# Performance work log

Measured on AMD Instinct MI355X. Metric: run time of the kernel, lower is better.

## Reference

```python
import jax, jax.numpy as jnp
import numpy as np
from jax import lax

B, T_IN, T_OUT = 32, 400, 500
N_MEL, ENC, RNN, PRE, ATT, LOC_F, LOC_K = 80, 512, 1024, 256, 128, 32, 31


def setup_inputs() -> dict:
    key = jax.random.key(0)
    ks = jax.random.split(key, 16)
    s = 0.02
    p = lambda i, sh: (jax.random.normal(ks[i], sh) * s).astype(jnp.float32)
    memory = jax.random.normal(ks[0], (B, T_IN, ENC), dtype=jnp.float32)
    decoder_inputs = jax.random.normal(ks[1], (B, N_MEL, T_OUT), dtype=jnp.float32)
    memory_lengths = jax.random.randint(ks[2], (B,), T_IN // 2, T_IN + 1).at[0].set(T_IN).astype(jnp.int32)
    return {
        'memory': memory,
        'decoder_inputs': decoder_inputs,
        'memory_lengths': memory_lengths,
        'prenet_w1': p(3, (PRE, N_MEL)),
        'prenet_w2': p(4, (PRE, PRE)),
        'att_wih': p(5, (4 * RNN, PRE + ENC)),
        'att_whh': p(6, (4 * RNN, RNN)),
        'att_bih': jnp.zeros((4 * RNN,), jnp.float32),
        'att_bhh': jnp.zeros((4 * RNN,), jnp.float32),
        'query_w': p(7, (ATT, RNN)),
        'memory_w': p(8, (ATT, ENC)),
        'v_w': p(9, (1, ATT)),
        'loc_conv_w': p(10, (LOC_F, 2, LOC_K)),
        'loc_lin_w': p(11, (ATT, LOC_F)),
        'dec_wih': p(12, (4 * RNN, RNN + ENC)),
        'dec_whh': p(13, (4 * RNN, RNN)),
        'dec_bih': jnp.zeros((4 * RNN,), jnp.float32),
        'dec_bhh': jnp.zeros((4 * RNN,), jnp.float32),
        'proj_w': p(14, (N_MEL, RNN + ENC)),
        'proj_b': jnp.zeros((N_MEL,), jnp.float32),
        'gate_w': p(15, (1, RNN + ENC)),
        'gate_b': jnp.zeros((1,), jnp.float32),
    }


def _lstm(x, h, c, wih, whh, bih, bhh):
    g = x @ wih.T + h @ whh.T + bih + bhh
    i, f, gg, o = jnp.split(g, 4, axis=-1)
    c2 = jax.nn.sigmoid(f) * c + jax.nn.sigmoid(i) * jnp.tanh(gg)
    return jax.nn.sigmoid(o) * jnp.tanh(c2), c2


def _forward(memory, decoder_inputs, memory_lengths, prenet_w1, prenet_w2,
             att_wih, att_whh, att_bih, att_bhh, query_w, memory_w, v_w,
             loc_conv_w, loc_lin_w, dec_wih, dec_whh, dec_bih, dec_bhh,
             proj_w, proj_b, gate_w, gate_b):
    # deterministic dropout masks (prenet p=0.5 always on; rnn dropout p=0.1, training mode)
    k1, k2, k3, k4 = jax.random.split(jax.random.key(42), 4)
    # teacher-forced inputs: [B,80,T_out] -> [T_out,B,80], prepend all-zero go frame
    dec_in = jnp.transpose(decoder_inputs, (2, 0, 1))
    dec_in = jnp.concatenate([jnp.zeros((1, B, N_MEL), decoder_inputs.dtype), dec_in], axis=0)
    x = dec_in
    for w, k in ((prenet_w1, k1), (prenet_w2, k2)):
        x = jax.nn.relu(x @ w.T)
        x = jnp.where(jax.random.bernoulli(k, 0.5, x.shape), x * 2.0, 0.0)
    prenet_out = x[:T_OUT]  # one decode step per target frame
    att_drop = jnp.where(jax.random.bernoulli(k3, 0.9, (T_OUT, B, RNN)), 1.0 / 0.9, 0.0).astype(jnp.float32)
    dec_drop = jnp.where(jax.random.bernoulli(k4, 0.9, (T_OUT, B, RNN)), 1.0 / 0.9, 0.0).astype(jnp.float32)
    processed_memory = memory @ memory_w.T  # [B,T_in,ATT]
    valid = jnp.arange(T_IN)[None, :] < memory_lengths[:, None]  # [B,T_in]
    pad = (LOC_K - 1) // 2

    def step(carry, xs):
        ah, ac, dh, dc, aw, awc, ctx = carry
        din, am, dm = xs
        ah, ac = _lstm(jnp.concatenate([din, ctx], -1), ah, ac, att_wih, att_whh, att_bih, att_bhh)
        ah = ah * am
        cat = jnp.stack([aw, awc], axis=1)  # [B,2,T_in]
        loc = lax.conv_general_dilated(cat, loc_conv_w, (1,), [(pad, pad)], dimension_numbers=('NCH', 'OIH', 'NCH'))
        loc = jnp.einsum('bft,af->bta', loc, loc_lin_w)  # [B,T_in,ATT]
        pq = (ah @ query_w.T)[:, None, :]  # [B,1,ATT]
        e = jnp.tanh(pq + loc + processed_memory) @ v_w[0]  # [B,T_in]
        e = jnp.where(valid, e, -jnp.inf)
        aw2 = jax.nn.softmax(e, axis=1)
        ctx2 = jnp.einsum('bt,btd->bd', aw2, memory)
        awc2 = awc + aw2
        dh, dc = _lstm(jnp.concatenate([ah, ctx2], -1), dh, dc, dec_wih, dec_whh, dec_bih, dec_bhh)
        dh = dh * dm
        hc = jnp.concatenate([dh, ctx2], -1)
        mel = hc @ proj_w.T + proj_b
        gate = (hc @ gate_w.T + gate_b)[:, 0]
        return (ah, ac, dh, dc, aw2, awc2, ctx2), (mel, gate, aw2)

    z = lambda *sh: jnp.zeros(sh, jnp.float32)
    carry0 = (z(B, RNN), z(B, RNN), z(B, RNN), z(B, RNN), z(B, T_IN), z(B, T_IN), z(B, ENC))
    _, (mels, gates, aligns) = lax.scan(step, carry0, (prenet_out, att_drop, dec_drop))
    mel_outputs = jnp.transpose(mels, (1, 2, 0))      # [B, n_mel, T_out]
    gate_outputs = gates.T                             # [B, T_out]
    alignments = jnp.transpose(aligns, (1, 0, 2))      # [B, T_out, T_in]
    return mel_outputs, gate_outputs, alignments


def reference(memory, decoder_inputs, memory_lengths, prenet_w1, prenet_w2,
              att_wih, att_whh, att_bih, att_bhh, query_w, memory_w, v_w,
              loc_conv_w, loc_lin_w, dec_wih, dec_whh, dec_bih, dec_bhh,
              proj_w, proj_b, gate_w, gate_b):
    return _forward(memory, decoder_inputs, memory_lengths, prenet_w1, prenet_w2,
                    att_wih, att_whh, att_bih, att_bhh, query_w, memory_w, v_w,
                    loc_conv_w, loc_lin_w, dec_wih, dec_whh, dec_bih, dec_bhh,
                    proj_w, proj_b, gate_w, gate_b)
```

## Files before the change

kernel.cpp:

```cpp
#include <hip/hip_runtime.h>
#include <cstdint>

typedef unsigned short ushortT;
typedef __attribute__((ext_vector_type(8))) short s8v;
typedef __attribute__((ext_vector_type(4))) float f4v;

#define TIN 400
#define TOUT 500

__host__ __device__ __forceinline__ uint32_t rotl32(uint32_t v, int r){ return (v<<r)|(v>>(32-r)); }
__host__ __device__ inline void tf2x32(uint32_t k0, uint32_t k1, uint32_t x0, uint32_t x1,
                                       uint32_t* o0, uint32_t* o1){
  uint32_t ks2 = k0 ^ k1 ^ 0x1BD11BDAu;
  x0 += k0; x1 += k1;
  x0+=x1; x1=rotl32(x1,13); x1^=x0;  x0+=x1; x1=rotl32(x1,15); x1^=x0;
  x0+=x1; x1=rotl32(x1,26); x1^=x0;  x0+=x1; x1=rotl32(x1, 6); x1^=x0;
  x0+=k1; x1+=ks2+1u;
  x0+=x1; x1=rotl32(x1,17); x1^=x0;  x0+=x1; x1=rotl32(x1,29); x1^=x0;
  x0+=x1; x1=rotl32(x1,16); x1^=x0;  x0+=x1; x1=rotl32(x1,24); x1^=x0;
  x0+=ks2; x1+=k0+2u;
  x0+=x1; x1=rotl32(x1,13); x1^=x0;  x0+=x1; x1=rotl32(x1,15); x1^=x0;
  x0+=x1; x1=rotl32(x1,26); x1^=x0;  x0+=x1; x1=rotl32(x1, 6); x1^=x0;
  x0+=k0; x1+=k1+3u;
  x0+=x1; x1=rotl32(x1,17); x1^=x0;  x0+=x1; x1=rotl32(x1,29); x1^=x0;
  x0+=x1; x1=rotl32(x1,16); x1^=x0;  x0+=x1; x1=rotl32(x1,24); x1^=x0;
  x0+=k1; x1+=ks2+4u;
  x0+=x1; x1=rotl32(x1,13); x1^=x0;  x0+=x1; x1=rotl32(x1,15); x1^=x0;
  x0+=x1; x1=rotl32(x1,26); x1^=x0;  x0+=x1; x1=rotl32(x1, 6); x1^=x0;
  x0+=ks2; x1+=k0+5u;
  *o0 = x0; *o1 = x1;
}
__device__ __forceinline__ float part_unif(uint32_t ka, uint32_t kb, uint32_t idx){
  uint32_t o0,o1; tf2x32(ka,kb,0u,idx,&o0,&o1);
  uint32_t bits = o0 ^ o1;
  return __uint_as_float(0x3f800000u | (bits>>9)) - 1.0f;
}

__device__ __forceinline__ float bf2f(ushortT u){ return __uint_as_float(((uint32_t)u)<<16); }
__device__ __forceinline__ ushortT f2bf(float f){
  uint32_t x = __float_as_uint(f);
  return (ushortT)((x + 0x7fffu + ((x>>16)&1u)) >> 16);
}
__device__ __forceinline__ float sigm(float x){ return 1.0f/(1.0f+__expf(-x)); }
__device__ __forceinline__ f4v mfma16(s8v a, s8v b, f4v c){
  return __builtin_amdgcn_mfma_f32_16x16x32_bf16(a,b,c,0,0,0);
}
__device__ __forceinline__ s8v pack8(const float* p){
  s8v r;
  #pragma unroll
  for (int j=0;j<8;++j) r[j]=(short)f2bf(p[j]);
  return r;
}

__global__ __launch_bounds__(256) void k_setup(
  const float* __restrict__ memory, const float* __restrict__ qw,
  const float* __restrict__ pjw,  const float* __restrict__ gw,
  ushortT* __restrict__ Mbf, ushortT* __restrict__ Wq, ushortT* __restrict__ Wpg,
  ushortT* __restrict__ AH0, ushortT* __restrict__ AH1,
  ushortT* __restrict__ DH0, ushortT* __restrict__ DH1,
  ushortT* __restrict__ CT0, ushortT* __restrict__ CT1,
  float* __restrict__ aw, float* __restrict__ awc,
  uint32_t* __restrict__ bars)
{
  int stride = gridDim.x*blockDim.x;
  int g0 = blockIdx.x*blockDim.x + threadIdx.x;
  for (int i=g0; i<32*400*512; i+=stride) Mbf[i]=f2bf(memory[i]);
  for (int i=g0; i<128*1024;  i+=stride) Wq[i]=f2bf(qw[i]);
  for (int i=g0; i<96*1536; i+=stride){
    int r=i/1536, k=i-r*1536;
    ushortT v=0;
    if (r<80) v=f2bf(pjw[r*1536+k]);
    else if (r==80) v=f2bf(gw[k]);
    Wpg[i]=v;
  }
  for (int i=g0; i<32*1024; i+=stride){ AH0[i]=0; AH1[i]=0; DH0[i]=0; DH1[i]=0; }
  for (int i=g0; i<32*512;  i+=stride){ CT0[i]=0; CT1[i]=0; }
  for (int i=g0; i<32*400;  i+=stride){ aw[i]=0.f; awc[i]=0.f; }
  if (g0 < 8) bars[g0]=0u;
}

__global__ __launch_bounds__(256) void k_prenet(
  const float* __restrict__ dec_inp, const float* __restrict__ w1, const float* __restrict__ w2,
  ushortT* __restrict__ preo,
  uint32_t k1a, uint32_t k1b, uint32_t k2a, uint32_t k2b)
{
  __shared__ ushortT Xs[64*96];
  __shared__ ushortT H1s[64*256];
  int tid=threadIdx.x, lane=tid&63, wv=tid>>6, quad=lane>>4, nl=lane&15;
  int r0 = blockIdx.x*64;
  for (int i=tid; i<64*96; i+=256){
    int rr=i/96, k=i-rr*96; int row=r0+rr; int s=row>>5, b=row&31;
    float v=0.f;
    if (k<80 && s>0) v = dec_inp[((size_t)b*80+k)*500 + (s-1)];
    Xs[i]=f2bf(v);
  }
  __syncthreads();
  f4v acc[4][4];
  #pragma unroll
  for (int mtl=0;mtl<4;++mtl)
    #pragma unroll
    for (int nt=0;nt<4;++nt) acc[mtl][nt]=(f4v){0,0,0,0};
  for (int kb=0;kb<3;++kb){
    int c0 = kb*32 + quad*8;
    s8v a[4];
    #pragma unroll
    for (int mtl=0;mtl<4;++mtl) a[mtl]=*(const s8v*)(Xs + (mtl*16+nl)*96 + c0);
    #pragma unroll
    for (int nt=0;nt<4;++nt){
      int rown = wv*64+nt*16+nl;
      s8v bb;
      if (c0 < 80) bb = pack8(w1 + (size_t)rown*80 + c0);
      else { s8v z={0,0,0,0,0,0,0,0}; bb=z; }
      #pragma unroll
      for (int mtl=0;mtl<4;++mtl) acc[mtl][nt]=mfma16(a[mtl],bb,acc[mtl][nt]);
    }
  }
  #pragma unroll
  for (int mtl=0;mtl<4;++mtl)
    #pragma unroll
    for (int nt=0;nt<4;++nt)
      #pragma unroll
      for (int r=0;r<4;++r){
        int mloc = mtl*16+quad*4+r;
        int col  = wv*64+nt*16+nl;
        float v = acc[mtl][nt][r]; v = v>0.f? v:0.f;
        uint32_t fidx = (uint32_t)(r0+mloc)*256u + (uint32_t)col;
        v = (part_unif(k1a,k1b,fidx) < 0.5f) ? v*2.0f : 0.0f;
        H1s[mloc*256+col]=f2bf(v);
      }
  __syncthreads();
  #pragma unroll
  for (int mtl=0;mtl<4;++mtl)
    #pragma unroll
    for (int nt=0;nt<4;++nt) acc[mtl][nt]=(f4v){0,0,0,0};
  for (int kb=0;kb<8;++kb){
    int c0 = kb*32 + quad*8;
    s8v a[4];
    #pragma unroll
    for (int mtl=0;mtl<4;++mtl) a[mtl]=*(const s8v*)(H1s + (mtl*16+nl)*256 + c0);
    #pragma unroll
    for (int nt=0;nt<4;++nt){
      int rown = wv*64+nt*16+nl;
      s8v bb = pack8(w2 + (size_t)rown*256 + c0);
      #pragma unroll
      for (int mtl=0;mtl<4;++mtl) acc[mtl][nt]=mfma16(a[mtl],bb,acc[mtl][nt]);
    }
  }
  #pragma unroll
  for (int mtl=0;mtl<4;++mtl)
    #pragma unroll
    for (int nt=0;nt<4;++nt)
      #pragma unroll
      for (int r=0;r<4;++r){
        int mloc = mtl*16+quad*4+r;
        int col  = wv*64+nt*16+nl;
        float v = acc[mtl][nt][r]; v = v>0.f? v:0.f;
        uint32_t fidx = (uint32_t)(r0+mloc)*256u + (uint32_t)col;
        v = (part_unif(k2a,k2b,fidx) < 0.5f) ? v*2.0f : 0.0f;
        preo[(size_t)(r0+mloc)*256+col]=f2bf(v);
      }
}

__global__ __launch_bounds__(256) void k_pm(
  const float* __restrict__ memory, const float* __restrict__ mw, float* __restrict__ pm)
{
  int row = blockIdx.x*2 + (threadIdx.x>>7);
  int col = threadIdx.x & 127;
  const float* mr = memory + (size_t)row*512;
  const float* wr = mw + (size_t)col*512;
  float acc=0.f;
  for (int k=0;k<512;k+=4){
    float4 a=*(const float4*)(mr+k), b=*(const float4*)(wr+k);
    acc += a.x*b.x + a.y*b.y + a.z*b.z + a.w*b.w;
  }
  pm[(size_t)row*128+col]=acc;
}

struct PArgs {
  const float* awih; const float* awhh; const float* abih; const float* abhh;
  const float* dwih; const float* dwhh; const float* dbih; const float* dbhh;
  const float* lcw;  const float* llw;  const float* vw;
  const float* pjb;  const float* gb;
  const float* pm;   const int* mlen;
  const ushortT* preo; const ushortT* Wq; const ushortT* Wpg; const ushortT* Mbf;
  ushortT* AH0; ushortT* AH1; ushortT* DH0; ushortT* DH1; ushortT* CT0; ushortT* CT1;
  float* aw; float* awc; float* ebuf;
  float* out_mel; float* out_gate; float* out_align;
  uint32_t* bars;
  uint32_t katt_a, katt_b, kdec_a, kdec_b;
};

__device__ __forceinline__ void gridbar(uint32_t* cnt, uint32_t* gen, uint32_t nb, uint32_t* myg){
  __syncthreads();
  if (threadIdx.x == 0){
    uint32_t g = *myg + 1u; *myg = g;
    __builtin_amdgcn_fence(__ATOMIC_RELEASE, "agent");
    uint32_t prev = __hip_atomic_fetch_add(cnt, 1u, __ATOMIC_RELAXED, __HIP_MEMORY_SCOPE_AGENT);
    if (prev == g*nb - 1u){
      __hip_atomic_store(gen, g, __ATOMIC_RELAXED, __HIP_MEMORY_SCOPE_AGENT);
    } else {
      while (__hip_atomic_load(gen, __ATOMIC_RELAXED, __HIP_MEMORY_SCOPE_AGENT) < g){
        __builtin_amdgcn_s_sleep(8);
      }
    }
    __builtin_amdgcn_fence(__ATOMIC_ACQUIRE, "agent");
  }
  __syncthreads();
}

__global__ __launch_bounds__(256,1) void k_persist(PArgs p){
  __shared__ ushortT Wa[16*1800];
  __shared__ ushortT Wd[16*2568];
  __shared__ float gbufA[2][16][33];
  __shared__ float gbufD[2][16][33];
  __shared__ float acst[4][32];
  __shared__ float dcst[4][32];
  __shared__ float biasA[16];
  __shared__ float biasD[16];
  __shared__ float sc[3400];

  const int tid = threadIdx.x;
  const int bid = blockIdx.x;
  const int lane = tid & 63;
  const int wv = tid >> 6;
  const int quad = lane >> 4;
  const int nl = lane & 15;
  const int mt = wv & 1;
  const int kh = wv >> 1;

  for (int rl=0; rl<16; ++rl){
    const int r = (rl>>2)*1024 + bid*4 + (rl&3);
    for (int c=tid; c<1792; c+=256){
      float v = (c<768) ? p.awih[(size_t)r*768+c] : p.awhh[(size_t)r*1024+(c-768)];
      Wa[rl*1800+c] = f2bf(v);
    }
    for (int c=tid; c<2560; c+=256){
      float v = (c<1536) ? p.dwih[(size_t)r*1536+c] : p.dwhh[(size_t)r*1024+(c-1536)];
      Wd[rl*2568+c] = f2bf(v);
    }
  }
  if (tid < 16){
    int g=tid>>2, u=bid*4+(tid&3);
    biasA[tid]=p.abih[g*1024+u]+p.abhh[g*1024+u];
    biasD[tid]=p.dbih[g*1024+u]+p.dbhh[g*1024+u];
  }
  if (tid < 128){ acst[tid>>5][tid&31]=0.f; dcst[tid>>5][tid&31]=0.f; }
  __syncthreads();

  uint32_t myg = 0;
  uint32_t* cnt = p.bars;
  uint32_t* gen = p.bars + 1;
  const uint32_t NB = gridDim.x;

  for (int t=0; t<=TOUT; ++t){
    const ushortT* AHp = (t&1)? p.AH0 : p.AH1;
    ushortT*       AHn = (t&1)? p.AH1 : p.AH0;
    const ushortT* DHi = (t&1)? p.DH1 : p.DH0;
    ushortT*       DHo = (t&1)? p.DH0 : p.DH1;
    const ushortT* CTXp= (t&1)? p.CT1 : p.CT0;
    ushortT*       CTXn= (t&1)? p.CT0 : p.CT1;

    const int arow = mt*16 + nl;
    if (t < TOUT){
      const ushortT* Xp = p.preo + ((size_t)t*32 + arow)*256 + quad*8;
      const ushortT* Xc = CTXp + arow*512 + quad*8;
      const ushortT* Xa = AHp + arow*1024 + quad*8;
      const ushortT* wr = Wa + nl*1800 + quad*8;
      f4v acc = {0.f,0.f,0.f,0.f};
      if (kh==0){
        #pragma unroll
        for (int kb=0;kb<8;++kb)  acc = mfma16(*(const s8v*)(Xp+kb*32), *(const s8v*)(wr+kb*32), acc);
        #pragma unroll
        for (int kb=0;kb<16;++kb) acc = mfma16(*(const s8v*)(Xc+kb*32), *(const s8v*)(wr+256+kb*32), acc);
        #pragma unroll
        for (int kb=0;kb<4;++kb)  acc = mfma16(*(const s8v*)(Xa+kb*32), *(const s8v*)(wr+768+kb*32), acc);
      } else {
        #pragma unroll
        for (int kb=0;kb<28;++kb) acc = mfma16(*(const s8v*)(Xa+128+kb*32), *(const s8v*)(wr+896+kb*32), acc);
      }
      #pragma unroll
      for (int r4=0;r4<4;++r4) gbufA[kh][nl][mt*16+quad*4+r4]=acc[r4];
    }
    if (t >= 1){
      const ushortT* Xa = AHp + arow*1024 + quad*8;
      const ushortT* Xc = CTXp + arow*512 + quad*8;
      const ushortT* Xd = DHi + arow*1024 + quad*8;
      const ushortT* wr = Wd + nl*2568 + quad*8;
      f4v acc = {0.f,0.f,0.f,0.f};
      if (kh==0){
        #pragma unroll
        for (int kb=0;kb<32;++kb) acc = mfma16(*(const s8v*)(Xa+kb*32), *(const s8v*)(wr+kb*32), acc);
        #pragma unroll
        for (int kb=0;kb<8;++kb)  acc = mfma16(*(const s8v*)(Xc+kb*32), *(const s8v*)(wr+1024+kb*32), acc);
      } else {
        #pragma unroll
        for (int kb=0;kb<8;++kb)  acc = mfma16(*(const s8v*)(Xc+256+kb*32), *(const s8v*)(wr+1280+kb*32), acc);
        #pragma unroll
        for (int kb=0;kb<32;++kb) acc = mfma16(*(const s8v*)(Xd+kb*32), *(const s8v*)(wr+1536+kb*32), acc);
      }
      #pragma unroll
      for (int r4=0;r4<4;++r4) gbufD[kh][nl][mt*16+quad*4+r4]=acc[r4];
    }
    __syncthreads();
    if (t < TOUT && tid < 128){
      const int uu=tid>>5, b=tid&31, u=bid*4+uu;
      float gi=gbufA[0][uu][b]   +gbufA[1][uu][b]   +biasA[uu];
      float gf=gbufA[0][4+uu][b] +gbufA[1][4+uu][b] +biasA[4+uu];
      float gg=gbufA[0][8+uu][b] +gbufA[1][8+uu][b] +biasA[8+uu];
      float go=gbufA[0][12+uu][b]+gbufA[1][12+uu][b]+biasA[12+uu];
      float cp=acst[uu][b];
      float c2=sigm(gf)*cp+sigm(gi)*tanhf(gg);
      float h =sigm(go)*tanhf(c2);
      uint32_t fidx=((uint32_t)(t*32+b))*1024u+(uint32_t)u;
      h=(part_unif(p.katt_a,p.katt_b,fidx)<0.9f)? h*(1.0f/0.9f):0.f;
      acst[uu][b]=c2;
      AHn[b*1024+u]=f2bf(h);
    }
    if (t >= 1 && tid >= 128){
      const int uu=(tid>>5)&3, b=tid&31, u=bid*4+uu;
      float gi=gbufD[0][uu][b]   +gbufD[1][uu][b]   +biasD[uu];
      float gf=gbufD[0][4+uu][b] +gbufD[1][4+uu][b] +biasD[4+uu];
      float gg=gbufD[0][8+uu][b] +gbufD[1][8+uu][b] +biasD[8+uu];
      float go=gbufD[0][12+uu][b]+gbufD[1][12+uu][b]+biasD[12+uu];
      float cp=dcst[uu][b];
      float c2=sigm(gf)*cp+sigm(gi)*tanhf(gg);
      float h =sigm(go)*tanhf(c2);
      uint32_t fidx=((uint32_t)((t-1)*32+b))*1024u+(uint32_t)u;
      h=(part_unif(p.kdec_a,p.kdec_b,fidx)<0.9f)? h*(1.0f/0.9f):0.f;
      dcst[uu][b]=c2;
      DHo[b*1024+u]=f2bf(h);
    }
    gridbar(cnt,gen,NB,&myg);

    if (bid < 128){
      if (t < TOUT){
        const int b = bid>>2, ch = bid&3, t0 = ch*100;
        float* xA = (float*)gbufA;
        float* xD = (float*)gbufD;
        ushortT* sAH = (ushortT*)xA;
        for (int i=tid;i<1024;i+=256) sAH[i]=AHn[b*1024+i];
        for (int i=tid;i<130;i+=256){
          int tt=t0-15+i; float a_=0.f,c_=0.f;
          if (tt>=0 && tt<TIN){ a_=p.aw[b*TIN+tt]; c_=p.awc[b*TIN+tt]; }
          xD[i]=a_; xD[130+i]=c_;
        }
        __syncthreads();
        {
          const int a=tid&127, half=tid>>7;
          const ushortT* qr = p.Wq + a*1024 + half*512;
          const ushortT* hr = sAH + half*512;
          float acc=0.f;
          for (int k=0;k<512;k+=8){
            s8v q=*(const s8v*)(qr+k);
            s8v h=*(const s8v*)(hr+k);
            #pragma unroll
            for (int j=0;j<8;++j) acc += bf2f((ushortT)q[j])*bf2f((ushortT)h[j]);
          }
          xA[512+tid]=acc;
        }
        for (int it=tid; it<3200; it+=256){
          const int tl=it>>5, f=it&31;
          const float* c0p=p.lcw + (f*2)*31;
          const float* c1p=c0p + 31;
          float s=0.f;
          #pragma unroll
          for (int j=0;j<31;++j) s += xD[tl+j]*c0p[j] + xD[130+tl+j]*c1p[j];
          sc[tl*32+f]=s;
        }
        __syncthreads();
        if (tid<128) xA[768+tid]=xA[512+tid]+xA[512+128+tid];
        __syncthreads();
        {
          const int a_=tid&127, g=tid>>7, wid=tid>>6;
          float lw_r[32];
          #pragma unroll
          for (int j=0;j<32;++j) lw_r[j]=p.llw[a_*32+j];
          const float vr = p.vw[a_];
          const float pqa = xA[768+a_];
          for (int tl=g; tl<100; tl+=2){
            const float* lt = sc + tl*32;
            float l2=0.f;
            #pragma unroll
            for (int f=0;f<32;++f) l2 += lt[f]*lw_r[f];
            float x = pqa + l2 + p.pm[((size_t)b*TIN + (t0+tl))*128 + a_];
            x = fminf(fmaxf(x,-30.f),30.f);
            float ex = __expf(2.f*x);
            float cv = vr*((ex-1.f)*__builtin_amdgcn_rcpf(ex+1.f));
            #pragma unroll
            for (int o=32;o>0;o>>=1) cv += __shfl_xor(cv,o);
            if ((tid&63)==0) xD[260 + tl*2 + (wid&1)]=cv;
          }
        }
        __syncthreads();
        if (tid<100){
          const int tg=t0+tid;
          float e = xD[260+tid*2] + xD[260+tid*2+1];
          float pv = (tg < p.mlen[b]) ? __expf(e) : 0.f;
          p.ebuf[b*TIN+tg]=pv;
        }
      }
    } else if (bid < 134){
      if (t >= 1){
        const int td=t-1, rb=(bid-128)*16;
        const int mrow = nl + mt*16;
        const ushortT* br  = p.Wpg + (size_t)(rb+nl)*1536 + quad*8;
        const ushortT* dhp = DHo + (size_t)mrow*1024 + quad*8;
        const ushortT* cxp = CTXp + (size_t)mrow*512 + quad*8;
        f4v acc={0.f,0.f,0.f,0.f};
        for (int kb=0;kb<24;++kb){
          const int kk=kh*768+kb*32;
          s8v aa = (kk<1024)? *(const s8v*)(dhp+kk) : *(const s8v*)(cxp+(kk-1024));
          acc = mfma16(aa, *(const s8v*)(br+kk), acc);
        }
        #pragma unroll
        for (int r4=0;r4<4;++r4) sc[kh*512 + (mt*16+quad*4+r4)*16 + nl]=acc[r4];
        __syncthreads();
        for (int idx=tid; idx<512; idx+=256){
          const int m=idx>>4, n=idx&15, r=rb+n;
          float v=sc[m*16+n]+sc[512+m*16+n];
          if (r<80) p.out_mel[(size_t)(m*80+r)*500+td]=v+p.pjb[r];
          else if (r==80) p.out_gate[(size_t)m*500+td]=v+p.gb[0];
        }
      }
    }
    gridbar(cnt,gen,NB,&myg);

    if (t < TOUT){
      const int b = bid>>3, s = bid&7;
      float* pv  = (float*)gbufA;
      float* red = pv + 408;
      for (int i=tid;i<TIN;i+=256) pv[i]=p.ebuf[b*TIN+i];
      __syncthreads();
      float ls=0.f;
      for (int i=tid;i<TIN;i+=256) ls+=pv[i];
      #pragma unroll
      for (int o=32;o>0;o>>=1) ls+=__shfl_xor(ls,o);
      if ((tid&63)==0) red[tid>>6]=ls;
      __syncthreads();
      const float S=red[0]+red[1]+red[2]+red[3];
      const float rS=(S>0.f)?1.0f/S:0.f;
      const int dl = tid&63, q = tid>>6;
      const int d = s*64 + dl;
      const ushortT* mb = p.Mbf + ((size_t)b*TIN + q*100)*512 + d;
      const float* pq_ = pv + q*100;
      float cc=0.f;
      #pragma unroll 4
      for (int tt=0;tt<100;++tt) cc += pq_[tt]*bf2f(mb[(size_t)tt*512]);
      sc[q*64+dl]=cc;
      __syncthreads();
      if (q==0){
        float v = sc[dl]+sc[64+dl]+sc[128+dl]+sc[192+dl];
        CTXn[b*512+d]=f2bf(v*rS);
      }
      if (s==0){
        for (int i=tid;i<TIN;i+=256){
          float a2 = pv[i]*rS;
          p.aw[b*TIN+i]=a2;
          p.awc[b*TIN+i]+=a2;
          p.out_align[((size_t)b*500+t)*400+i]=a2;
        }
      }
    }
    gridbar(cnt,gen,NB,&myg);
  }
}

extern "C" void kernel_launch(void* const* d_in, const int* in_sizes, int n_in,
                              void* d_out, int out_size, void* d_ws, size_t ws_size,
                              hipStream_t stream) {
  (void)in_sizes; (void)n_in; (void)out_size; (void)ws_size;
  const float* memory  = (const float*)d_in[0];
  const float* dec_inp = (const float*)d_in[1];
  const int*   mlen    = (const int*)d_in[2];
  const float* pw1     = (const float*)d_in[3];
  const float* pw2     = (const float*)d_in[4];
  const float* awih    = (const float*)d_in[5];
  const float* awhh    = (const float*)d_in[6];
  const float* abih    = (const float*)d_in[7];
  const float* abhh    = (const float*)d_in[8];
  const float* qw      = (const float*)d_in[9];
  const float* mw      = (const float*)d_in[10];
  const float* vw      = (const float*)d_in[11];
  const float* lcw     = (const float*)d_in[12];
  const float* llw     = (const float*)d_in[13];
  const float* dwih    = (const float*)d_in[14];
  const float* dwhh    = (const float*)d_in[15];
  const float* dbih    = (const float*)d_in[16];
  const float* dbhh    = (const float*)d_in[17];
  const float* pjw     = (const float*)d_in[18];
  const float* pjb     = (const float*)d_in[19];
  const float* gw      = (const float*)d_in[20];
  const float* gb      = (const float*)d_in[21];

  char* w = (char*)d_ws;
  size_t off=0;
  auto alloc = [&](size_t n)->char*{ char* p=w+off; off=(off+n+255)&~(size_t)255; return p; };
  ushortT* Mbf = (ushortT*)alloc(32UL*400*512*2);
  ushortT* Wq  = (ushortT*)alloc(128UL*1024*2);
  ushortT* Wpg = (ushortT*)alloc(96UL*1536*2);
  ushortT* preo= (ushortT*)alloc(16000UL*256*2);
  float*   pm  = (float*)alloc(12800UL*128*4);
  ushortT* AH0 = (ushortT*)alloc(32UL*1024*2);
  ushortT* AH1 = (ushortT*)alloc(32UL*1024*2);
  ushortT* DH0 = (ushortT*)alloc(32UL*1024*2);
  ushortT* DH1 = (ushortT*)alloc(32UL*1024*2);
  ushortT* CT0 = (ushortT*)alloc(32UL*512*2);
  ushortT* CT1 = (ushortT*)alloc(32UL*512*2);
  float*   aw  = (float*)alloc(12800UL*4);
  float*   awc = (float*)alloc(12800UL*4);
  float*   ebuf= (float*)alloc(12800UL*4);
  uint32_t* bars=(uint32_t*)alloc(256);

  uint32_t K[4][2];
  for (uint32_t i=0;i<4;++i) tf2x32(0u,42u,0u,i,&K[i][0],&K[i][1]);

  float* out_mel   = (float*)d_out;
  float* out_gate  = out_mel + 1280000;
  float* out_align = out_mel + 1296000;

  k_setup<<<1024,256,0,stream>>>(memory,qw,pjw,gw,Mbf,Wq,Wpg,AH0,AH1,DH0,DH1,CT0,CT1,aw,awc,bars);
  k_prenet<<<250,256,0,stream>>>(dec_inp, pw1, pw2, preo, K[0][0],K[0][1], K[1][0],K[1][1]);
  k_pm<<<6400,256,0,stream>>>(memory, mw, pm);

  PArgs pa;
  pa.awih=awih; pa.awhh=awhh; pa.abih=abih; pa.abhh=abhh;
  pa.dwih=dwih; pa.dwhh=dwhh; pa.dbih=dbih; pa.dbhh=dbhh;
  pa.lcw=lcw; pa.llw=llw; pa.vw=vw; pa.pjb=pjb; pa.gb=gb;
  pa.pm=pm; pa.mlen=mlen;
  pa.preo=preo; pa.Wq=Wq; pa.Wpg=Wpg; pa.Mbf=Mbf;
  pa.AH0=AH0; pa.AH1=AH1; pa.DH0=DH0; pa.DH1=DH1; pa.CT0=CT0; pa.CT1=CT1;
  pa.aw=aw; pa.awc=awc; pa.ebuf=ebuf;
  pa.out_mel=out_mel; pa.out_gate=out_gate; pa.out_align=out_align;
  pa.bars=bars;
  pa.katt_a=K[2][0]; pa.katt_b=K[2][1]; pa.kdec_a=K[3][0]; pa.kdec_b=K[3][1];

  void* kargs[] = { &pa };
  (void)hipLaunchCooperativeKernel((const void*)k_persist, dim3(256), dim3(256), kargs, 0u, stream);
}
```

Measured before the change: 50.64 ms.

## Use hierarchical grid barrier and drop acquire fence via agent-scope atomic loads

Replaces the single-counter grid barrier with a two-level counter tree (8 group counters padded to separate cache lines, plus a master counter), and shortens the spin sleep. The acquire fence after the barrier is removed. Loads of cross-block data (hidden states, context, attention weights, energies) now go through relaxed agent-scope atomic loads so they bypass stale cache lines without a full cache invalidation. This aims to cut per-step barrier latency across the roughly 1500 barriers. It hardcodes 256 blocks (32 per group × 8 groups) and relies on per-load coherence for correctness.

```diff
diff --git a/kernel.cpp b/kernel.cpp
--- a/kernel.cpp
+++ b/kernel.cpp
@@ -51,6 +51,18 @@
   for (int j=0;j<8;++j) r[j]=(short)f2bf(p[j]);
   return r;
 }
+__device__ __forceinline__ uint32_t ld32_sc1(const void* ptr){
+  return __hip_atomic_load((uint32_t*)ptr, __ATOMIC_RELAXED, __HIP_MEMORY_SCOPE_AGENT);
+}
+__device__ __forceinline__ float ldf_sc1(const float* ptr){
+  return __uint_as_float(ld32_sc1(ptr));
+}
+__device__ __forceinline__ s8v ld8_sc1(const ushortT* ptr){
+  union { s8v v; unsigned long long q[2]; } u;
+  u.q[0] = __hip_atomic_load((unsigned long long*)ptr,     __ATOMIC_RELAXED, __HIP_MEMORY_SCOPE_AGENT);
+  u.q[1] = __hip_atomic_load((unsigned long long*)ptr + 1, __ATOMIC_RELAXED, __HIP_MEMORY_SCOPE_AGENT);
+  return u.v;
+}
 
 __global__ __launch_bounds__(256) void k_setup(
   const float* __restrict__ memory, const float* __restrict__ qw,
@@ -76,7 +88,7 @@
   for (int i=g0; i<32*1024; i+=stride){ AH0[i]=0; AH1[i]=0; DH0[i]=0; DH1[i]=0; }
   for (int i=g0; i<32*512;  i+=stride){ CT0[i]=0; CT1[i]=0; }
   for (int i=g0; i<32*400;  i+=stride){ aw[i]=0.f; awc[i]=0.f; }
-  if (g0 < 8) bars[g0]=0u;
+  if (g0 < 512) bars[g0]=0u;
 }
 
 __global__ __launch_bounds__(256) void k_prenet(
@@ -190,20 +202,28 @@
   uint32_t katt_a, katt_b, kdec_a, kdec_b;
 };
 
-__device__ __forceinline__ void gridbar(uint32_t* cnt, uint32_t* gen, uint32_t nb, uint32_t* myg){
+__device__ __forceinline__ void gridbar(uint32_t* bars, uint32_t* myg){
   __syncthreads();
   if (threadIdx.x == 0){
     uint32_t g = *myg + 1u; *myg = g;
     __builtin_amdgcn_fence(__ATOMIC_RELEASE, "agent");
-    uint32_t prev = __hip_atomic_fetch_add(cnt, 1u, __ATOMIC_RELAXED, __HIP_MEMORY_SCOPE_AGENT);
-    if (prev == g*nb - 1u){
-      __hip_atomic_store(gen, g, __ATOMIC_RELAXED, __HIP_MEMORY_SCOPE_AGENT);
-    } else {
+    uint32_t* gc  = bars + 32u*(blockIdx.x & 7u);
+    uint32_t* mc  = bars + 256u;
+    uint32_t* gen = bars + 288u;
+    uint32_t prev = __hip_atomic_fetch_add(gc,1u,__ATOMIC_RELAXED,__HIP_MEMORY_SCOPE_AGENT);
+    bool setter=false;
+    if (prev == g*32u - 1u){
+      uint32_t p2 = __hip_atomic_fetch_add(mc,1u,__ATOMIC_RELAXED,__HIP_MEMORY_SCOPE_AGENT);
+      if (p2 == g*8u - 1u){
+        __hip_atomic_store(gen, g, __ATOMIC_RELAXED, __HIP_MEMORY_SCOPE_AGENT);
+        setter=true;
+      }
+    }
+    if (!setter){
       while (__hip_atomic_load(gen, __ATOMIC_RELAXED, __HIP_MEMORY_SCOPE_AGENT) < g){
-        __builtin_amdgcn_s_sleep(8);
-      }
-    }
-    __builtin_amdgcn_fence(__ATOMIC_ACQUIRE, "agent");
+        __builtin_amdgcn_s_sleep(2);
+      }
+    }
   }
   __syncthreads();
 }
@@ -248,9 +268,6 @@
   __syncthreads();
 
   uint32_t myg = 0;
-  uint32_t* cnt = p.bars;
-  uint32_t* gen = p.bars + 1;
-  const uint32_t NB = gridDim.x;
 
   for (int t=0; t<=TOUT; ++t){
     const ushortT* AHp = (t&1)? p.AH0 : p.AH1;
@@ -271,12 +288,12 @@
         #pragma unroll
         for (int kb=0;kb<8;++kb)  acc = mfma16(*(const s8v*)(Xp+kb*32), *(const s8v*)(wr+kb*32), acc);
         #pragma unroll
-        for (int kb=0;kb<16;++kb) acc = mfma16(*(const s8v*)(Xc+kb*32), *(const s8v*)(wr+256+kb*32), acc);
-        #pragma unroll
-        for (int kb=0;kb<4;++kb)  acc = mfma16(*(const s8v*)(Xa+kb*32), *(const s8v*)(wr+768+kb*32), acc);
+        for (int kb=0;kb<16;++kb) acc = mfma16(ld8_sc1(Xc+kb*32), *(const s8v*)(wr+256+kb*32), acc);
+        #pragma unroll
+        for (int kb=0;kb<4;++kb)  acc = mfma16(ld8_sc1(Xa+kb*32), *(const s8v*)(wr+768+kb*32), acc);
       } else {
         #pragma unroll
-        for (int kb=0;kb<28;++kb) acc = mfma16(*(const s8v*)(Xa+128+kb*32), *(const s8v*)(wr+896+kb*32), acc);
+        for (int kb=0;kb<28;++kb) acc = mfma16(ld8_sc1(Xa+128+kb*32), *(const s8v*)(wr+896+kb*32), acc);
       }
       #pragma unroll
       for (int r4=0;r4<4;++r4) gbufA[kh][nl][mt*16+quad*4+r4]=acc[r4];
@@ -289,14 +306,14 @@
       f4v acc = {0.f,0.f,0.f,0.f};
       if (kh==0){
         #pragma unroll
-        for (int kb=0;kb<32;++kb) acc = mfma16(*(const s8v*)(Xa+kb*32), *(const s8v*)(wr+kb*32), acc);
-        #pragma unroll
-        for (int kb=0;kb<8;++kb)  acc = mfma16(*(const s8v*)(Xc+kb*32), *(const s8v*)(wr+1024+kb*32), acc);
+        for (int kb=0;kb<32;++kb) acc = mfma16(ld8_sc1(Xa+kb*32), *(const s8v*)(wr+kb*32), acc);
+        #pragma unroll
+        for (int kb=0;kb<8;++kb)  acc = mfma16(ld8_sc1(Xc+kb*32), *(const s8v*)(wr+1024+kb*32), acc);
       } else {
         #pragma unroll
-        for (int kb=0;kb<8;++kb)  acc = mfma16(*(const s8v*)(Xc+256+kb*32), *(const s8v*)(wr+1280+kb*32), acc);
-        #pragma unroll
-        for (int kb=0;kb<32;++kb) acc = mfma16(*(const s8v*)(Xd+kb*32), *(const s8v*)(wr+1536+kb*32), acc);
+        for (int kb=0;kb<8;++kb)  acc = mfma16(ld8_sc1(Xc+256+kb*32), *(const s8v*)(wr+1280+kb*32), acc);
+        #pragma unroll
+        for (int kb=0;kb<32;++kb) acc = mfma16(ld8_sc1(Xd+kb*32), *(const s8v*)(wr+1536+kb*32), acc);
       }
       #pragma unroll
       for (int r4=0;r4<4;++r4) gbufD[kh][nl][mt*16+quad*4+r4]=acc[r4];
@@ -330,7 +347,7 @@
       dcst[uu][b]=c2;
       DHo[b*1024+u]=f2bf(h);
     }
-    gridbar(cnt,gen,NB,&myg);
+    gridbar(p.bars,&myg);
 
     if (bid < 128){
       if (t < TOUT){
@@ -338,10 +355,13 @@
         float* xA = (float*)gbufA;
         float* xD = (float*)gbufD;
         ushortT* sAH = (ushortT*)xA;
-        for (int i=tid;i<1024;i+=256) sAH[i]=AHn[b*1024+i];
+        {
+          const uint32_t* ahsrc = (const uint32_t*)(AHn + b*1024);
+          for (int i=tid;i<512;i+=256) ((uint32_t*)sAH)[i] = ld32_sc1(ahsrc + i);
+        }
         for (int i=tid;i<130;i+=256){
           int tt=t0-15+i; float a_=0.f,c_=0.f;
-          if (tt>=0 && tt<TIN){ a_=p.aw[b*TIN+tt]; c_=p.awc[b*TIN+tt]; }
+          if (tt>=0 && tt<TIN){ a_=ldf_sc1(p.aw + b*TIN+tt); c_=ldf_sc1(p.awc + b*TIN+tt); }
           xD[i]=a_; xD[130+i]=c_;
         }
         __syncthreads();
@@ -409,7 +429,7 @@
         f4v acc={0.f,0.f,0.f,0.f};
         for (int kb=0;kb<24;++kb){
           const int kk=kh*768+kb*32;
-          s8v aa = (kk<1024)? *(const s8v*)(dhp+kk) : *(const s8v*)(cxp+(kk-1024));
+          s8v aa = (kk<1024)? ld8_sc1(dhp+kk) : ld8_sc1(cxp+(kk-1024));
           acc = mfma16(aa, *(const s8v*)(br+kk), acc);
         }
         #pragma unroll
@@ -423,13 +443,13 @@
         }
       }
     }
-    gridbar(cnt,gen,NB,&myg);
+    gridbar(p.bars,&myg);
 
     if (t < TOUT){
       const int b = bid>>3, s = bid&7;
       float* pv  = (float*)gbufA;
       float* red = pv + 408;
-      for (int i=tid;i<TIN;i+=256) pv[i]=p.ebuf[b*TIN+i];
+      for (int i=tid;i<TIN;i+=256) pv[i]=ldf_sc1(p.ebuf + b*TIN + i);
       __syncthreads();
       float ls=0.f;
       for (int i=tid;i<TIN;i+=256) ls+=pv[i];
@@ -461,7 +481,7 @@
         }
       }
     }
-    gridbar(cnt,gen,NB,&myg);
+    gridbar(p.bars,&myg);
   }
 }
 
@@ -509,7 +529,7 @@
   float*   aw  = (float*)alloc(12800UL*4);
   float*   awc = (float*)alloc(12800UL*4);
   float*   ebuf= (float*)alloc(12800UL*4);
-  uint32_t* bars=(uint32_t*)alloc(256);
+  uint32_t* bars=(uint32_t*)alloc(2048);
 
   uint32_t K[4][2];
   for (uint32_t i=0;i<4;++i) tf2x32(0u,42u,0u,i,&K[i][0],&K[i][1]);
```

Result: faster. 42.15 ms (-16.8%).
